# Kernel optimization log

Measured on AMD Instinct MI355X. Metric: run time of the kernel, lower is better.

Reference implementation:

```python
import jax, jax.numpy as jnp
import numpy as np


def _lstm_layer(x_seq, h0, c0, Wih, Whh, bih, bhh):
    """Standard (PyTorch-gate-order: i, f, g, o) LSTM over a [T, B, C] sequence."""
    b = bih + bhh  # [4H]
    # Precompute input projections for all timesteps at once: [T, B, 4H]
    x_proj = jnp.einsum('tbc,gc->tbg', x_seq, Wih) + b

    def step(carry, xp_t):
        h, c = carry
        gates = xp_t + h @ Whh.T  # [B, 4H]
        i, f, g, o = jnp.split(gates, 4, axis=-1)
        i = jax.nn.sigmoid(i)
        f = jax.nn.sigmoid(f)
        g = jnp.tanh(g)
        o = jax.nn.sigmoid(o)
        c_new = f * c + i * g
        h_new = o * jnp.tanh(c_new)
        return (h_new, c_new), h_new

    (hT, cT), ys = jax.lax.scan(step, (h0, c0), x_proj)
    return ys, hT, cT


def setup_inputs() -> dict:
    key = jax.random.key(0)
    ks = jax.random.split(key, 16)
    T, B, C, H = 1024, 64, 256, 512
    s_in = 1.0 / np.sqrt(H)
    inp = {
        'x': jax.random.normal(ks[0], (T, B, C), jnp.float32),
        'h0_0': jax.random.normal(ks[1], (B, H), jnp.float32) * 0.1,
        'c0_0': jax.random.normal(ks[2], (B, H), jnp.float32) * 0.1,
        'h0_1': jax.random.normal(ks[3], (B, H), jnp.float32) * 0.1,
        'c0_1': jax.random.normal(ks[4], (B, H), jnp.float32) * 0.1,
        'Wih0': jax.random.normal(ks[5], (4 * H, C), jnp.float32) * s_in,
        'Whh0': jax.random.normal(ks[6], (4 * H, H), jnp.float32) * s_in,
        'bih0': jax.random.normal(ks[7], (4 * H,), jnp.float32) * s_in,
        'bhh0': jax.random.normal(ks[8], (4 * H,), jnp.float32) * s_in,
        'Wih1': jax.random.normal(ks[9], (4 * H, H), jnp.float32) * s_in,
        'Whh1': jax.random.normal(ks[10], (4 * H, H), jnp.float32) * s_in,
        'bih1': jax.random.normal(ks[11], (4 * H,), jnp.float32) * s_in,
        'bhh1': jax.random.normal(ks[12], (4 * H,), jnp.float32) * s_in,
    }
    return inp


def reference(x, h0_0, c0_0, h0_1, c0_1, Wih0, Whh0, bih0, bhh0, Wih1, Whh1, bih1, bhh1):
    # Layer 0 over the full sequence, then layer 1 consumes its outputs.
    # Mathematically identical to the original timestep-major Python loop.
    y0, h1f, c1f = _lstm_layer(x, h0_0, c0_0, Wih0, Whh0, bih0, bhh0)
    y1, h2f, c2f = _lstm_layer(y0, h0_1, c0_1, Wih1, Whh1, bih1, bhh1)
    return (y1, h1f, c1f, h2f, c2f)
```

## Files before the change

### kernel.cpp

```cpp
#include <hip/hip_runtime.h>


#define TT 1024
#define BB 64
#define CC 256
#define HH 512
#define Y_ELEMS (TT * BB * HH)
#define S_ELEMS (BB * HH)

typedef __attribute__((ext_vector_type(8))) short bf16x8;
typedef __attribute__((ext_vector_type(4))) float f32x4;
typedef unsigned int u32;
typedef unsigned short u16;
typedef unsigned long long u64;

#define WS_BAR 0
#define WS_CNT 32768
#define WS_BSUM0 36864
#define WS_BSUM1 45056
#define WS_H0 53248
#define WS_H1 184320
#define WS_WPK0 315392
#define WS_WPK1 3461120

__device__ __forceinline__ u16 f2b_rne(float f) {
    u32 u = __float_as_uint(f);
    return (u16)((u + 0x7FFFu + ((u >> 16) & 1u)) >> 16);
}
__device__ __forceinline__ u16 f2b_fast(float f) {
    return (u16)((__float_as_uint(f) + 0x8000u) >> 16);
}
__device__ __forceinline__ float sigf(float z) { return 1.0f / (1.0f + __expf(-z)); }
__device__ __forceinline__ float tanh_f(float z) { return 2.0f / (1.0f + __expf(-2.0f * z)) - 1.0f; }

__device__ __forceinline__ bf16x8 pack8(float4 a, float4 b) {
    union { u16 u[8]; bf16x8 v; } r;
    r.u[0] = f2b_fast(a.x); r.u[1] = f2b_fast(a.y); r.u[2] = f2b_fast(a.z); r.u[3] = f2b_fast(a.w);
    r.u[4] = f2b_fast(b.x); r.u[5] = f2b_fast(b.y); r.u[6] = f2b_fast(b.z); r.u[7] = f2b_fast(b.w);
    return r.v;
}

__device__ __forceinline__ u32 ld_u32_sc(const u32* p) {
    return __hip_atomic_load(p, __ATOMIC_RELAXED, __HIP_MEMORY_SCOPE_AGENT);
}
__device__ __forceinline__ void add_u32_sc(u32* p, u32 v) {
    (void)__hip_atomic_fetch_add(p, v, __ATOMIC_RELAXED, __HIP_MEMORY_SCOPE_AGENT);
}

__global__ void k_init(const float* __restrict__ bih0, const float* __restrict__ bhh0,
                       const float* __restrict__ bih1, const float* __restrict__ bhh1,
                       const float* __restrict__ h00, const float* __restrict__ h01,
                       unsigned char* __restrict__ ws) {
    u32* bar = (u32*)(ws + WS_BAR);
    float* bs0 = (float*)(ws + WS_BSUM0);
    float* bs1 = (float*)(ws + WS_BSUM1);
    u16* h0 = (u16*)(ws + WS_H0);
    u16* h1 = (u16*)(ws + WS_H1);
    int t = blockIdx.x * 256 + threadIdx.x;
    if (t < 8448) bar[t] = 0u;
    if (t < 2048) { bs0[t] = bih0[t] + bhh0[t]; bs1[t] = bih1[t] + bhh1[t]; }
    if (t < S_ELEMS) {
        int b = t >> 9, col = t & 511;
        int no = ((col >> 2) << 8) + (b << 2) + (col & 3);
        h0[no] = f2b_rne(h00[t]);
        h1[no] = f2b_rne(h01[t]);
    }
}

__global__ void k_wprep(const float* __restrict__ Wih0, const float* __restrict__ Whh0,
                        const float* __restrict__ Wih1, const float* __restrict__ Whh1,
                        unsigned char* __restrict__ ws) {
    u16* wpk0 = (u16*)(ws + WS_WPK0);
    u16* wpk1 = (u16*)(ws + WS_WPK1);
    int u = blockIdx.x * 256 + threadIdx.x;
    const float* s;
    u16* d;
    if (u < 128 * 24 * 64) {
        int bidL = u / (24 * 64);
        int kt = (u >> 6) % 24;
        int lane = u & 63;
        int n = lane & 15, quad = lane >> 4;
        int row = (n >> 2) * 512 + bidL * 4 + (n & 3);
        int k = kt * 32 + quad * 8;
        s = (k < 256) ? (Wih0 + (size_t)row * 256 + k) : (Whh0 + (size_t)row * 512 + (k - 256));
        d = wpk0 + (size_t)((bidL * 24 + kt) * 64 + lane) * 8;
    } else {
        int v = u - 128 * 24 * 64;
        int bidL = v / (32 * 64);
        int kt = (v >> 6) % 32;
        int lane = v & 63;
        int n = lane & 15, quad = lane >> 4;
        int row = (n >> 2) * 512 + bidL * 4 + (n & 3);
        int k = kt * 32 + quad * 8;
        s = (k < 512) ? (Wih1 + (size_t)row * 512 + k) : (Whh1 + (size_t)row * 512 + (k - 512));
        d = wpk1 + (size_t)((bidL * 32 + kt) * 64 + lane) * 8;
    }
    #pragma unroll
    for (int i = 0; i < 8; ++i) d[i] = f2b_rne(s[i]);
}

template <int LAYER>
__device__ void run_ticks(const float* __restrict__ x, const float* __restrict__ c0,
                          float* __restrict__ out, unsigned char* __restrict__ ws, int bidL) {
    constexpr int NKT = (LAYER == 0) ? 24 : 32;
    u32* cnt = (u32*)(ws + WS_CNT);
    const float* bs = (const float*)(ws + (LAYER == 0 ? WS_BSUM0 : WS_BSUM1));
    u16* h0base = (u16*)(ws + WS_H0);
    u16* h1base = (u16*)(ws + WS_H1);
    const u16* wpk = (const u16*)(ws + (LAYER == 0 ? WS_WPK0 : WS_WPK1));

    const int tid = threadIdx.x, lane = tid & 63, wave = tid >> 6;
    const int r16 = lane & 15, quad = lane >> 4, q8 = quad * 8;
    const int gg = r16 >> 2, jj = r16 & 3;
    const int b0 = wave * 16;
    const int col = bidL * 4 + jj;
    const int myb = b0 + quad * 4 + gg;
    const int sl0 = (quad << 4) | (0 << 2) | jj;
    const int sl1 = (quad << 4) | (1 << 2) | jj;
    const int sl2 = (quad << 4) | (2 << 2) | jj;
    const int sl3 = (quad << 4) | (3 << 2) | jj;
    const int baseln = (quad << 4) | (gg << 2);

    const size_t cbase = (size_t)quad * 1024 + (size_t)(b0 + r16) * 8;

    u32* mycnt = cnt + ((u32)blockIdx.x & 7) * 32;

    const float bi = bs[0 * HH + col], bf_ = bs[1 * HH + col];
    const float bg = bs[2 * HH + col], bo = bs[3 * HH + col];
    float c = c0[myb * HH + col];

    f32x4 wf[NKT];
    {
        const u16* wp = wpk + (size_t)(bidL * NKT * 64 + lane) * 8;
        #pragma unroll
        for (int kt = 0; kt < NKT; ++kt) wf[kt] = *(const f32x4*)(wp + (size_t)kt * 64 * 8);
        #pragma unroll
        for (int kt = 0; kt < NKT; ++kt) asm volatile("" : "+v"(wf[kt]));
    }

    float4 xf0[8], xf1[8];
    if (LAYER == 0) {
        const float* xp = x + (size_t)(b0 + r16) * CC + q8;
        #pragma unroll
        for (int kt = 0; kt < 8; ++kt) {
            xf0[kt] = *(const float4*)(xp + kt * 32);
            xf1[kt] = *(const float4*)(xp + kt * 32 + 4);
        }
    }

    for (int i = 0; i <= TT; ++i) {
        const bool active = (LAYER == 0) ? (i < TT) : (i >= 1);
        const int t = (LAYER == 0) ? i : i - 1;
        float h = 0.f;
        if (active) {
            f32x4 a0 = {0.f,0.f,0.f,0.f}, a1 = {0.f,0.f,0.f,0.f};
            f32x4 a2 = {0.f,0.f,0.f,0.f}, a3 = {0.f,0.f,0.f,0.f};
            if (LAYER == 0) {
                u64 alo[16], ahi[16];
                {
                    const char* hb = (const char*)(h0base + (size_t)(t & 1) * S_ELEMS) + cbase;
                    #pragma unroll
                    for (int kt = 0; kt < 16; ++kt) {
                        const char* pk = hb + kt * 4096;
                        asm volatile("global_load_dwordx2 %0, %1, off sc0 sc1"
                                     : "=&v"(alo[kt]) : "v"(pk) : "memory");
                        asm volatile("global_load_dwordx2 %0, %1, off offset:512 sc0 sc1"
                                     : "=&v"(ahi[kt]) : "v"(pk) : "memory");
                    }
                }
                #pragma unroll
                for (int kt = 0; kt < 8; ++kt) {
                    bf16x8 a = pack8(xf0[kt], xf1[kt]);
                    bf16x8 wv = __builtin_bit_cast(bf16x8, wf[kt]);
                    f32x4& dst = (kt & 2) ? ((kt & 1) ? a3 : a2) : ((kt & 1) ? a1 : a0);
                    dst = __builtin_amdgcn_mfma_f32_16x16x32_bf16(a, wv, dst, 0, 0, 0);
                }
                asm volatile("s_waitcnt vmcnt(0)" ::: "memory");
                __builtin_amdgcn_sched_barrier(0);
                #pragma unroll
                for (int kt = 0; kt < 16; ++kt) {
                    union { u64 q[2]; bf16x8 v; } fa;
                    fa.q[0] = alo[kt]; fa.q[1] = ahi[kt];
                    bf16x8 wv = __builtin_bit_cast(bf16x8, wf[8 + kt]);
                    f32x4& dst = (kt & 2) ? ((kt & 1) ? a3 : a2) : ((kt & 1) ? a1 : a0);
                    dst = __builtin_amdgcn_mfma_f32_16x16x32_bf16(fa.v, wv, dst, 0, 0, 0);
                }
            } else {
                u64 plo[16], phi[16], qlo[16], qhi[16];
                {
                    const char* ha = (const char*)(h0base + (size_t)((t + 1) & 1) * S_ELEMS) + cbase;
                    const char* hb = (const char*)(h1base + (size_t)(t & 1) * S_ELEMS) + cbase;
                    #pragma unroll
                    for (int kt = 0; kt < 16; ++kt) {
                        const char* pk = hb + kt * 4096;
                        asm volatile("global_load_dwordx2 %0, %1, off sc0 sc1"
                                     : "=&v"(qlo[kt]) : "v"(pk) : "memory");
                        asm volatile("global_load_dwordx2 %0, %1, off offset:512 sc0 sc1"
                                     : "=&v"(qhi[kt]) : "v"(pk) : "memory");
                    }
                    #pragma unroll
                    for (int kt = 0; kt < 16; ++kt) {
                        const char* pk = ha + kt * 4096;
                        asm volatile("global_load_dwordx2 %0, %1, off sc0 sc1"
                                     : "=&v"(plo[kt]) : "v"(pk) : "memory");
                        asm volatile("global_load_dwordx2 %0, %1, off offset:512 sc0 sc1"
                                     : "=&v"(phi[kt]) : "v"(pk) : "memory");
                    }
                }
                asm volatile("s_waitcnt vmcnt(32)" ::: "memory");
                __builtin_amdgcn_sched_barrier(0);
                #pragma unroll
                for (int kt = 16; kt < 32; ++kt) {
                    union { u64 q[2]; bf16x8 v; } fa;
                    fa.q[0] = qlo[kt - 16]; fa.q[1] = qhi[kt - 16];
                    bf16x8 wv = __builtin_bit_cast(bf16x8, wf[kt]);
                    f32x4& dst = (kt & 2) ? ((kt & 1) ? a3 : a2) : ((kt & 1) ? a1 : a0);
                    dst = __builtin_amdgcn_mfma_f32_16x16x32_bf16(fa.v, wv, dst, 0, 0, 0);
                }
                asm volatile("s_waitcnt vmcnt(0)" ::: "memory");
                __builtin_amdgcn_sched_barrier(0);
                #pragma unroll
                for (int kt = 0; kt < 16; ++kt) {
                    union { u64 q[2]; bf16x8 v; } fa;
                    fa.q[0] = plo[kt]; fa.q[1] = phi[kt];
                    bf16x8 wv = __builtin_bit_cast(bf16x8, wf[kt]);
                    f32x4& dst = (kt & 2) ? ((kt & 1) ? a3 : a2) : ((kt & 1) ? a1 : a0);
                    dst = __builtin_amdgcn_mfma_f32_16x16x32_bf16(fa.v, wv, dst, 0, 0, 0);
                }
            }
            f32x4 acc = (a0 + a1) + (a2 + a3);

            float gi = 0.f, gf = 0.f, gc = 0.f, go = 0.f;
            #pragma unroll
            for (int r = 0; r < 4; ++r) {
                float v0 = __shfl(acc[r], sl0, 64);
                float v1 = __shfl(acc[r], sl1, 64);
                float v2 = __shfl(acc[r], sl2, 64);
                float v3 = __shfl(acc[r], sl3, 64);
                if (r == gg) { gi = v0; gf = v1; gc = v2; go = v3; }
            }
            gi = sigf(gi + bi);
            gf = sigf(gf + bf_);
            gc = tanh_f(gc + bg);
            go = sigf(go + bo);
            c = gf * c + gi * gc;
            h = go * tanh_f(c);

            u32 w0 = f2b_rne(h);
            u32 w1 = (u32)__shfl((int)w0, baseln + 1, 64);
            u32 w2 = (u32)__shfl((int)w0, baseln + 2, 64);
            u32 w3 = (u32)__shfl((int)w0, baseln + 3, 64);
            if (jj == 0) {
                u64 pkd = (u64)(w0 | (w1 << 16)) | ((u64)(w2 | (w3 << 16)) << 32);
                u64* hw = (u64*)((LAYER == 0 ? h0base : h1base)
                                 + (size_t)((t + 1) & 1) * S_ELEMS)
                          + (size_t)bidL * 64 + myb;
                __hip_atomic_store(hw, pkd, __ATOMIC_RELAXED, __HIP_MEMORY_SCOPE_AGENT);
            }
        }
        if (i < TT) {
            asm volatile("s_waitcnt vmcnt(0)" ::: "memory");
            __syncthreads();
            if (tid == 0) add_u32_sc(mycnt, 1u);
        }
        if (active) {
            if (LAYER == 1) {
                float o1 = __shfl(h, baseln + 1, 64);
                float o2 = __shfl(h, baseln + 2, 64);
                float o3 = __shfl(h, baseln + 3, 64);
                if (jj == 0) {
                    float4 ov = { h, o1, o2, o3 };
                    *(float4*)(out + (size_t)t * S_ELEMS + (size_t)myb * HH + bidL * 4) = ov;
                }
            }
            if (t == TT - 1) {
                float* fin = out + Y_ELEMS + (LAYER == 0 ? 0 : 2) * S_ELEMS;
                fin[myb * HH + col] = h;
                fin[S_ELEMS + myb * HH + col] = c;
            }
        }
        if (LAYER == 0 && i + 1 < TT) {
            const float* xp = x + ((size_t)(i + 1) * BB + b0 + r16) * CC + q8;
            #pragma unroll
            for (int kt = 0; kt < 8; ++kt) {
                xf0[kt] = *(const float4*)(xp + kt * 32);
                xf1[kt] = *(const float4*)(xp + kt * 32 + 4);
            }
        }
        if (i < TT) {
            const u32 tgt = (u32)(i + 1) * 32u;
            if (tid == 0) {
                while (true) {
                    u32 v0 = ld_u32_sc(cnt + 0 * 32);
                    u32 v1 = ld_u32_sc(cnt + 1 * 32);
                    u32 v2 = ld_u32_sc(cnt + 2 * 32);
                    u32 v3 = ld_u32_sc(cnt + 3 * 32);
                    u32 v4 = ld_u32_sc(cnt + 4 * 32);
                    u32 v5 = ld_u32_sc(cnt + 5 * 32);
                    u32 v6 = ld_u32_sc(cnt + 6 * 32);
                    u32 v7 = ld_u32_sc(cnt + 7 * 32);
                    u32 m = min(min(min(v0, v1), min(v2, v3)),
                                min(min(v4, v5), min(v6, v7)));
                    if (m >= tgt) break;
                }
            }
            __syncthreads();
        }
    }
}

__global__ __launch_bounds__(256) __attribute__((amdgpu_waves_per_eu(1, 1)))
void k_lstm(const float* __restrict__ x,
            const float* __restrict__ c00,
            const float* __restrict__ c01,
            float* __restrict__ out,
            unsigned char* __restrict__ ws) {
    const int bid = blockIdx.x;
    if (bid < 128) run_ticks<0>(x, c00, out, ws, bid);
    else           run_ticks<1>(x, c01, out, ws, bid - 128);
}

extern "C" void kernel_launch(void* const* d_in, const int* in_sizes, int n_in,
                              void* d_out, int out_size, void* d_ws, size_t ws_size,
                              hipStream_t stream) {
    const float* x    = (const float*)d_in[0];
    const float* h0_0 = (const float*)d_in[1];
    const float* c0_0 = (const float*)d_in[2];
    const float* h0_1 = (const float*)d_in[3];
    const float* c0_1 = (const float*)d_in[4];
    const float* Wih0 = (const float*)d_in[5];
    const float* Whh0 = (const float*)d_in[6];
    const float* bih0 = (const float*)d_in[7];
    const float* bhh0 = (const float*)d_in[8];
    const float* Wih1 = (const float*)d_in[9];
    const float* Whh1 = (const float*)d_in[10];
    const float* bih1 = (const float*)d_in[11];
    const float* bhh1 = (const float*)d_in[12];
    float* out = (float*)d_out;
    unsigned char* ws = (unsigned char*)d_ws;

    k_init<<<128, 256, 0, stream>>>(bih0, bhh0, bih1, bhh1, h0_0, h0_1, ws);
    k_wprep<<<1792, 256, 0, stream>>>(Wih0, Whh0, Wih1, Whh1, ws);
    k_lstm<<<256, 256, 0, stream>>>(x, c0_0, c0_1, out, ws);
}
```

Measured before the change: 4.984 ms.

## Repartition blocks by batch-group and column-group, staging hidden state through LDS

```diff
diff --git a/kernel.cpp b/kernel.cpp
--- a/kernel.cpp
+++ b/kernel.cpp
@@ -61,7 +61,7 @@
     if (t < 2048) { bs0[t] = bih0[t] + bhh0[t]; bs1[t] = bih1[t] + bhh1[t]; }
     if (t < S_ELEMS) {
         int b = t >> 9, col = t & 511;
-        int no = ((col >> 2) << 8) + (b << 2) + (col & 3);
+        int no = ((col >> 4) << 10) + (b << 4) + (col & 15);
         h0[no] = f2b_rne(h00[t]);
         h1[no] = f2b_rne(h01[t]);
     }
@@ -101,37 +101,42 @@
 
 template <int LAYER>
 __device__ void run_ticks(const float* __restrict__ x, const float* __restrict__ c0,
-                          float* __restrict__ out, unsigned char* __restrict__ ws, int bidL) {
+                          float* __restrict__ out, unsigned char* __restrict__ ws,
+                          int bidL, unsigned char* lds) {
     constexpr int NKT = (LAYER == 0) ? 24 : 32;
+    constexpr int NL = (LAYER == 0) ? 4 : 8;
     u32* cnt = (u32*)(ws + WS_CNT);
     const float* bs = (const float*)(ws + (LAYER == 0 ? WS_BSUM0 : WS_BSUM1));
     u16* h0base = (u16*)(ws + WS_H0);
     u16* h1base = (u16*)(ws + WS_H1);
     const u16* wpk = (const u16*)(ws + (LAYER == 0 ? WS_WPK0 : WS_WPK1));
 
+    const int bg = bidL >> 5;
+    const int cg = bidL & 31;
     const int tid = threadIdx.x, lane = tid & 63, wave = tid >> 6;
     const int r16 = lane & 15, quad = lane >> 4, q8 = quad * 8;
     const int gg = r16 >> 2, jj = r16 & 3;
-    const int b0 = wave * 16;
-    const int col = bidL * 4 + jj;
-    const int myb = b0 + quad * 4 + gg;
+    const int col = cg * 16 + wave * 4 + jj;
+    const int mb = quad * 4 + gg;
+    const int myb = bg * 16 + mb;
     const int sl0 = (quad << 4) | (0 << 2) | jj;
     const int sl1 = (quad << 4) | (1 << 2) | jj;
     const int sl2 = (quad << 4) | (2 << 2) | jj;
     const int sl3 = (quad << 4) | (3 << 2) | jj;
     const int baseln = (quad << 4) | (gg << 2);
 
-    const size_t cbase = (size_t)quad * 1024 + (size_t)(b0 + r16) * 8;
+    u16* hstage = (u16*)(lds + 32768);
+    const int sw = (r16 & 7) << 4;
 
     u32* mycnt = cnt + ((u32)blockIdx.x & 7) * 32;
 
     const float bi = bs[0 * HH + col], bf_ = bs[1 * HH + col];
-    const float bg = bs[2 * HH + col], bo = bs[3 * HH + col];
+    const float bg_ = bs[2 * HH + col], bo = bs[3 * HH + col];
     float c = c0[myb * HH + col];
 
     f32x4 wf[NKT];
     {
-        const u16* wp = wpk + (size_t)(bidL * NKT * 64 + lane) * 8;
+        const u16* wp = wpk + (size_t)((cg * 4 + wave) * NKT * 64 + lane) * 8;
         #pragma unroll
         for (int kt = 0; kt < NKT; ++kt) wf[kt] = *(const f32x4*)(wp + (size_t)kt * 64 * 8);
         #pragma unroll
@@ -140,7 +145,7 @@
 
     float4 xf0[8], xf1[8];
     if (LAYER == 0) {
-        const float* xp = x + (size_t)(b0 + r16) * CC + q8;
+        const float* xp = x + (size_t)(bg * 16 + r16) * CC + q8;
         #pragma unroll
         for (int kt = 0; kt < 8; ++kt) {
             xf0[kt] = *(const float4*)(xp + kt * 32);
@@ -153,21 +158,24 @@
         const int t = (LAYER == 0) ? i : i - 1;
         float h = 0.f;
         if (active) {
+            f32x4 stg[NL];
+            {
+                const char* srcA = (const char*)(h0base + (size_t)((LAYER == 0 ? t : t + 1) & 1) * S_ELEMS);
+                const char* srcB = (const char*)(h1base + (size_t)(t & 1) * S_ELEMS);
+                #pragma unroll
+                for (int k = 0; k < NL; ++k) {
+                    int g = (k & 3) * 4096 + tid * 16;
+                    int cgi = g >> 9;
+                    int off = g & 511;
+                    const char* sp = ((LAYER == 1 && k >= 4) ? srcB : srcA)
+                                   + (size_t)cgi * 2048 + bg * 512 + off;
+                    asm volatile("global_load_dwordx4 %0, %1, off sc0 sc1"
+                                 : "=&v"(stg[k]) : "v"(sp) : "memory");
+                }
+            }
             f32x4 a0 = {0.f,0.f,0.f,0.f}, a1 = {0.f,0.f,0.f,0.f};
             f32x4 a2 = {0.f,0.f,0.f,0.f}, a3 = {0.f,0.f,0.f,0.f};
             if (LAYER == 0) {
-                u64 alo[16], ahi[16];
-                {
-                    const char* hb = (const char*)(h0base + (size_t)(t & 1) * S_ELEMS) + cbase;
-                    #pragma unroll
-                    for (int kt = 0; kt < 16; ++kt) {
-                        const char* pk = hb + kt * 4096;
-                        asm volatile("global_load_dwordx2 %0, %1, off sc0 sc1"
-                                     : "=&v"(alo[kt]) : "v"(pk) : "memory");
-                        asm volatile("global_load_dwordx2 %0, %1, off offset:512 sc0 sc1"
-                                     : "=&v"(ahi[kt]) : "v"(pk) : "memory");
-                    }
-                }
                 #pragma unroll
                 for (int kt = 0; kt < 8; ++kt) {
                     bf16x8 a = pack8(xf0[kt], xf1[kt]);
@@ -175,57 +183,55 @@
                     f32x4& dst = (kt & 2) ? ((kt & 1) ? a3 : a2) : ((kt & 1) ? a1 : a0);
                     dst = __builtin_amdgcn_mfma_f32_16x16x32_bf16(a, wv, dst, 0, 0, 0);
                 }
-                asm volatile("s_waitcnt vmcnt(0)" ::: "memory");
-                __builtin_amdgcn_sched_barrier(0);
+            }
+            asm volatile("s_waitcnt vmcnt(0)" ::: "memory");
+            #pragma unroll
+            for (int k = 0; k < NL; ++k) {
+                int g = (k & 3) * 4096 + tid * 16;
+                int cgi = g >> 9;
+                int off = g & 511;
+                int m = off >> 5;
+                int lo = (cgi * 32 + (off & 16)) ^ ((m & 7) << 4);
+                int base = (LAYER == 1 && k >= 4) ? 16384 : 0;
+                *(f32x4*)(lds + base + m * 1024 + lo) = stg[k];
+            }
+            __syncthreads();
+            if (LAYER == 0) {
                 #pragma unroll
-                for (int kt = 0; kt < 16; ++kt) {
-                    union { u64 q[2]; bf16x8 v; } fa;
-                    fa.q[0] = alo[kt]; fa.q[1] = ahi[kt];
-                    bf16x8 wv = __builtin_bit_cast(bf16x8, wf[8 + kt]);
-                    f32x4& dst = (kt & 2) ? ((kt & 1) ? a3 : a2) : ((kt & 1) ? a1 : a0);
-                    dst = __builtin_amdgcn_mfma_f32_16x16x32_bf16(fa.v, wv, dst, 0, 0, 0);
-                }
-            } else {
-                u64 plo[16], phi[16], qlo[16], qhi[16];
-                {
-                    const char* ha = (const char*)(h0base + (size_t)((t + 1) & 1) * S_ELEMS) + cbase;
-                    const char* hb = (const char*)(h1base + (size_t)(t & 1) * S_ELEMS) + cbase;
+                for (int kc = 0; kc < 16; kc += 8) {
+                    bf16x8 av[8];
                     #pragma unroll
-                    for (int kt = 0; kt < 16; ++kt) {
-                        const char* pk = hb + kt * 4096;
-                        asm volatile("global_load_dwordx2 %0, %1, off sc0 sc1"
-                                     : "=&v"(qlo[kt]) : "v"(pk) : "memory");
-                        asm volatile("global_load_dwordx2 %0, %1, off offset:512 sc0 sc1"
-                                     : "=&v"(qhi[kt]) : "v"(pk) : "memory");
+                    for (int j = 0; j < 8; ++j) {
+                        int kt = kc + j;
+                        int lo2 = (kt * 64 + quad * 16) ^ sw;
+                        av[j] = *(const bf16x8*)(lds + r16 * 1024 + lo2);
                     }
                     #pragma unroll
-                    for (int kt = 0; kt < 16; ++kt) {
-                        const char* pk = ha + kt * 4096;
-                        asm volatile("global_load_dwordx2 %0, %1, off sc0 sc1"
-                                     : "=&v"(plo[kt]) : "v"(pk) : "memory");
-                        asm volatile("global_load_dwordx2 %0, %1, off offset:512 sc0 sc1"
-                                     : "=&v"(phi[kt]) : "v"(pk) : "memory");
+                    for (int j = 0; j < 8; ++j) {
+                        int kt = kc + j;
+                        bf16x8 wv = __builtin_bit_cast(bf16x8, wf[8 + kt]);
+                        f32x4& dst = (kt & 2) ? ((kt & 1) ? a3 : a2) : ((kt & 1) ? a1 : a0);
+                        dst = __builtin_amdgcn_mfma_f32_16x16x32_bf16(av[j], wv, dst, 0, 0, 0);
                     }
                 }
-                asm volatile("s_waitcnt vmcnt(32)" ::: "memory");
-                __builtin_amdgcn_sched_barrier(0);
+            } else {
                 #pragma unroll
-                for (int kt = 16; kt < 32; ++kt) {
-                    union { u64 q[2]; bf16x8 v; } fa;
-                    fa.q[0] = qlo[kt - 16]; fa.q[1] = qhi[kt - 16];
-                    bf16x8 wv = __builtin_bit_cast(bf16x8, wf[kt]);
-                    f32x4& dst = (kt & 2) ? ((kt & 1) ? a3 : a2) : ((kt & 1) ? a1 : a0);
-                    dst = __builtin_amdgcn_mfma_f32_16x16x32_bf16(fa.v, wv, dst, 0, 0, 0);
-                }
-                asm volatile("s_waitcnt vmcnt(0)" ::: "memory");
-                __builtin_amdgcn_sched_barrier(0);
-                #pragma unroll
-                for (int kt = 0; kt < 16; ++kt) {
-                    union { u64 q[2]; bf16x8 v; } fa;
-                    fa.q[0] = plo[kt]; fa.q[1] = phi[kt];
-                    bf16x8 wv = __builtin_bit_cast(bf16x8, wf[kt]);
-                    f32x4& dst = (kt & 2) ? ((kt & 1) ? a3 : a2) : ((kt & 1) ? a1 : a0);
-                    dst = __builtin_amdgcn_mfma_f32_16x16x32_bf16(fa.v, wv, dst, 0, 0, 0);
+                for (int kc = 0; kc < 32; kc += 8) {
+                    bf16x8 av[8];
+                    #pragma unroll
+                    for (int j = 0; j < 8; ++j) {
+                        int kt = kc + j;
+                        int base = (kt < 16) ? 0 : 16384;
+                        int lo2 = ((kt & 15) * 64 + quad * 16) ^ sw;
+                        av[j] = *(const bf16x8*)(lds + base + r16 * 1024 + lo2);
+                    }
+                    #pragma unroll
+                    for (int j = 0; j < 8; ++j) {
+                        int kt = kc + j;
+                        bf16x8 wv = __builtin_bit_cast(bf16x8, wf[kt]);
+                        f32x4& dst = (kt & 2) ? ((kt & 1) ? a3 : a2) : ((kt & 1) ? a1 : a0);
+                        dst = __builtin_amdgcn_mfma_f32_16x16x32_bf16(av[j], wv, dst, 0, 0, 0);
+                    }
                 }
             }
             f32x4 acc = (a0 + a1) + (a2 + a3);
@@ -241,7 +247,7 @@
             }
             gi = sigf(gi + bi);
             gf = sigf(gf + bf_);
-            gc = tanh_f(gc + bg);
+            gc = tanh_f(gc + bg_);
             go = sigf(go + bo);
             c = gf * c + gi * gc;
             h = go * tanh_f(c);
@@ -252,13 +258,18 @@
             u32 w3 = (u32)__shfl((int)w0, baseln + 3, 64);
             if (jj == 0) {
                 u64 pkd = (u64)(w0 | (w1 << 16)) | ((u64)(w2 | (w3 << 16)) << 32);
-                u64* hw = (u64*)((LAYER == 0 ? h0base : h1base)
-                                 + (size_t)((t + 1) & 1) * S_ELEMS)
-                          + (size_t)bidL * 64 + myb;
-                __hip_atomic_store(hw, pkd, __ATOMIC_RELAXED, __HIP_MEMORY_SCOPE_AGENT);
+                *(u64*)((char*)hstage + mb * 32 + wave * 8) = pkd;
             }
         }
         if (i < TT) {
+            __syncthreads();
+            if (active && tid < 32) {
+                u16* hw = (LAYER == 0 ? h0base : h1base) + (size_t)((t + 1) & 1) * S_ELEMS;
+                f32x4 v = *(const f32x4*)((const char*)hstage + tid * 16);
+                const char* dp = (const char*)hw + (size_t)cg * 2048 + bg * 512 + tid * 16;
+                asm volatile("global_store_dwordx4 %0, %1, off sc0 sc1"
+                             :: "v"(dp), "v"(v) : "memory");
+            }
             asm volatile("s_waitcnt vmcnt(0)" ::: "memory");
             __syncthreads();
             if (tid == 0) add_u32_sc(mycnt, 1u);
@@ -270,7 +281,8 @@
                 float o3 = __shfl(h, baseln + 3, 64);
                 if (jj == 0) {
                     float4 ov = { h, o1, o2, o3 };
-                    *(float4*)(out + (size_t)t * S_ELEMS + (size_t)myb * HH + bidL * 4) = ov;
+                    *(float4*)(out + (size_t)t * S_ELEMS + (size_t)myb * HH
+                               + cg * 16 + wave * 4) = ov;
                 }
             }
             if (t == TT - 1) {
@@ -280,7 +292,7 @@
             }
         }
         if (LAYER == 0 && i + 1 < TT) {
-            const float* xp = x + ((size_t)(i + 1) * BB + b0 + r16) * CC + q8;
+            const float* xp = x + ((size_t)(i + 1) * BB + bg * 16 + r16) * CC + q8;
             #pragma unroll
             for (int kt = 0; kt < 8; ++kt) {
                 xf0[kt] = *(const float4*)(xp + kt * 32);
@@ -315,9 +327,10 @@
             const float* __restrict__ c01,
             float* __restrict__ out,
             unsigned char* __restrict__ ws) {
+    __shared__ __align__(16) unsigned char lds[33280];
     const int bid = blockIdx.x;
-    if (bid < 128) run_ticks<0>(x, c00, out, ws, bid);
-    else           run_ticks<1>(x, c01, out, ws, bid - 128);
+    if (bid < 128) run_ticks<0>(x, c00, out, ws, bid, lds);
+    else           run_ticks<1>(x, c01, out, ws, bid - 128, lds);
 }
 
 extern "C" void kernel_launch(void* const* d_in, const int* in_sizes, int n_in,
```

Result: faster. 4.717 ms (-5.4%).
